# Kernel tuning notes

Measured on AMD Instinct MI355X. Metric: run time of the kernel, lower is better.

## Reference

```python
import jax, jax.numpy as jnp
import numpy as np

HIND = 512
D = 256
P = 512          # 2*d Givens rotations
RHO_MAX = 9.0
DELTA = 1e-3
EPS = 1e-8
B = 32768


def setup_inputs() -> dict:
    key = jax.random.key(0)
    ks = jax.random.split(key, 12)
    f = lambda k, shape, sc=1.0: jax.random.normal(k, shape, dtype=jnp.float32) * sc
    return {
        "ent_embed": f(ks[0], (B, HIND)),
        "rel_embed": f(ks[1], (B, HIND)),
        "ent_label": f(ks[2], (B, HIND)),
        "sim": jax.random.uniform(ks[3], (B,), dtype=jnp.float32),
        # W_v: Linear(hind, d)
        "Wv": f(ks[4], (D, HIND), 0.05), "bv": jnp.zeros((D,), jnp.float32),
        # w_rho_ent: Linear(hind, 1), bias init 0.5
        "Wre": f(ks[5], (1, HIND), 0.05), "bre": jnp.full((1,), 0.5, jnp.float32),
        # w_rho_rel: Linear(hind, 1)
        "Wrr": f(ks[6], (1, HIND), 0.05), "brr": jnp.zeros((1,), jnp.float32),
        # W_theta: Linear(hind, P)
        "Wt": f(ks[7], (P, HIND), 0.05), "bt": jnp.zeros((P,), jnp.float32),
        "ga_rho": jnp.array([2.0], jnp.float32), "gb_rho": jnp.array([-0.5], jnp.float32),
        "ga_phi": jnp.array([2.0], jnp.float32), "gb_phi": jnp.array([-0.5], jnp.float32),
        # pre_mlp: Linear(hind,hind) -> ReLU -> Linear(hind,hind)
        "W1": f(ks[8], (HIND, HIND), 0.03), "b1": jnp.zeros((HIND,), jnp.float32),
        "W2": f(ks[9], (HIND, HIND), 0.03), "b2": jnp.zeros((HIND,), jnp.float32),
    }


def _l2norm(x):
    return x / (jnp.linalg.norm(x, axis=1, keepdims=True) + EPS)


def _forward(ent_embed, rel_embed, ent_label, sim,
             Wv, bv, Wre, bre, Wrr, brr, Wt, bt,
             ga_rho, gb_rho, ga_phi, gb_phi, W1, b1, W2, b2):
    pre = lambda x: x + jax.nn.relu(x @ W1.T + b1) @ W2.T + b2  # residual pre_mlp
    E_h, E_r, E_t = pre(ent_embed), pre(rel_embed), pre(ent_label)

    def to_polar(E):
        u = _l2norm(E @ Wv.T + bv)                       # [B, D] direction
        rho = jax.nn.softplus(E @ Wre.T + bre)           # [B, 1] radius
        return jnp.clip(rho, 0.0, RHO_MAX), u

    rho_h, u_h = to_polar(E_h)
    delta_rho = E_r @ Wrr.T + brr                        # [B, 1]
    thetas = jnp.pi * jnp.tanh(E_r @ Wt.T + bt)          # [B, P]

    simc = sim.reshape(-1, 1)
    g_rho = jax.nn.sigmoid(ga_rho * simc + gb_rho)
    g_phi = jax.nn.sigmoid(ga_phi * simc + gb_phi)
    rho_prime = jnp.clip(rho_h + delta_rho * g_rho, 0.0, RHO_MAX)

    # Sequential Givens rotations: pairs (m % D, (m % D + 1) % D)
    ii = jnp.arange(P, dtype=jnp.int32) % D
    jj = (ii + 1) % D
    c = jnp.cos(thetas).T                                # [P, B]
    s = jnp.sin(thetas).T

    def step(out, t):
        i, j, cm, sm = t
        ui, uj = out[:, i], out[:, j]
        out = out.at[:, i].set(cm * ui - sm * uj)
        out = out.at[:, j].set(sm * ui + cm * uj)
        return out, None

    u_rot, _ = jax.lax.scan(step, u_h, (ii, jj, c, s))
    u_rot = _l2norm(u_rot)

    # slerp(u_h -> u_rot, alpha = g_phi), lerp fallback when omega <= DELTA
    dot = jnp.clip(jnp.sum(u_h * u_rot, axis=1, keepdims=True), -1.0 + EPS, 1.0 - EPS)
    omega = jnp.arccos(dot)
    sin_omega = jnp.sin(omega)
    mask = (omega > DELTA).astype(u_h.dtype)
    s1 = jnp.sin((1.0 - g_phi) * omega) / (sin_omega + EPS)
    s2 = jnp.sin(g_phi * omega) / (sin_omega + EPS)
    u_prime = mask * (s1 * u_h + s2 * u_rot) + (1.0 - mask) * ((1.0 - g_phi) * u_h + g_phi * u_rot)
    u_prime = _l2norm(u_prime)

    rho_t, u_t = to_polar(E_t)
    # Lorentz lift: X = [cosh(rho), sinh(rho)*u]; inner = -x0*y0 + <xs, ys>
    Xh0, Xhs = jnp.cosh(rho_prime), jnp.sinh(rho_prime) * u_prime
    Xt0, Xts = jnp.cosh(rho_t), jnp.sinh(rho_t) * u_t
    score = (-Xh0 * Xt0 + jnp.sum(Xhs * Xts, axis=1, keepdims=True))[:, 0]  # [B]
    return score


def reference(ent_embed, rel_embed, ent_label, sim,
              Wv, bv, Wre, bre, Wrr, brr, Wt, bt,
              ga_rho, gb_rho, ga_phi, gb_phi, W1, b1, W2, b2):
    return _forward(ent_embed, rel_embed, ent_label, sim,
                    Wv, bv, Wre, bre, Wrr, brr, Wt, bt,
                    ga_rho, gb_rho, ga_phi, gb_phi, W1, b1, W2, b2)
```

## Files before the change

kernel.cpp:

```cpp
#include <hip/hip_runtime.h>
#include <cstdint>

#define NB 32768
#define HH 512

typedef __attribute__((ext_vector_type(8))) _Float16 f16x8;
typedef __attribute__((ext_vector_type(4))) float f32x4;
typedef __attribute__((ext_vector_type(4))) unsigned short us4v;

__device__ __forceinline__ unsigned short f2h(float f) {
  _Float16 h = (_Float16)f;
  return __builtin_bit_cast(unsigned short, h);
}
__device__ __forceinline__ float h2f(unsigned short u) {
  return (float)__builtin_bit_cast(_Float16, u);
}

__device__ __forceinline__ void gl_lds16(const void* g, void* l) {
  __builtin_amdgcn_global_load_lds(
      (const __attribute__((address_space(1))) unsigned int*)g,
      (__attribute__((address_space(3))) unsigned int*)l, 16, 0, 0);
}

__device__ __forceinline__ float wred(float v) {
#pragma unroll
  for (int off = 32; off > 0; off >>= 1) v += __shfl_xor(v, off);
  return v;
}

__device__ __forceinline__ float softplusf(float x) {
  return fmaxf(x, 0.f) + log1pf(expf(-fabsf(x)));
}

__global__ __launch_bounds__(256) void prep_w(
    const float* __restrict__ W1, const float* __restrict__ W2,
    const float* __restrict__ Wv, const float* __restrict__ Wt,
    unsigned short* __restrict__ W1h, unsigned short* __restrict__ W2h,
    unsigned short* __restrict__ Wvh, unsigned short* __restrict__ Wth,
    float* __restrict__ rho) {
  int i = blockIdx.x * 256 + threadIdx.x;
  if (i < 98304) rho[i] = 0.f;
  if (i < 262144) W1h[i] = f2h(W1[i]);
  else if (i < 524288) W2h[i - 262144] = f2h(W2[i - 262144]);
  else if (i < 655360) Wvh[i - 524288] = f2h(Wv[i - 524288]);
  else Wth[i - 655360] = f2h(Wt[i - 655360]);
}

__global__ __launch_bounds__(256) void gemm0_k(
    const float* __restrict__ A, const unsigned short* __restrict__ W,
    const float* __restrict__ bias, unsigned short* __restrict__ Out) {
  __shared__ float Af[128 * 64];
  __shared__ unsigned short Bs[128 * 64];
  const int tid = threadIdx.x, lane = tid & 63, w = tid >> 6;
  const long m0 = (long)blockIdx.y * 128;
  const int n0 = blockIdx.x * 128;
  const int wr = (w >> 1) * 64, wc = (w & 1) * 64;

  const int arow = w * 32 + (lane >> 4), acol = (lane & 15) * 4;
  const float* Ag = A + (long)(m0 + arow) * HH + acol;
  float* Al = Af + arow * 64 + acol;
  const int brow = w * 32 + (lane >> 3), bcol = (lane & 7) * 8;
  const unsigned short* Bg = W + (long)(n0 + brow) * HH + bcol;
  unsigned short* Bl = Bs + brow * 64 + bcol;

  f32x4 acc[4][4] = {};
  for (int kb = 0; kb < 8; ++kb) {
    const int ko = kb * 64;
#pragma unroll
    for (int q = 0; q < 8; ++q)
      gl_lds16(Ag + (long)(4 * q) * HH + ko, Al + (4 * q) * 64);
#pragma unroll
    for (int q = 0; q < 4; ++q)
      gl_lds16(Bg + (long)(8 * q) * HH + ko, Bl + (8 * q) * 64);
    __syncthreads();
#pragma unroll
    for (int ks = 0; ks < 2; ++ks) {
      const int kcol = ks * 32 + (lane >> 4) * 8;
      f16x8 af[4], bf[4];
#pragma unroll
      for (int i = 0; i < 4; ++i) {
        const float* ap = Af + (wr + i * 16 + (lane & 15)) * 64 + kcol;
        f32x4 a0 = *(const f32x4*)ap;
        f32x4 a1 = *(const f32x4*)(ap + 4);
        f16x8 t;
        t[0] = (_Float16)a0[0]; t[1] = (_Float16)a0[1];
        t[2] = (_Float16)a0[2]; t[3] = (_Float16)a0[3];
        t[4] = (_Float16)a1[0]; t[5] = (_Float16)a1[1];
        t[6] = (_Float16)a1[2]; t[7] = (_Float16)a1[3];
        af[i] = t;
        bf[i] = *(const f16x8*)(Bs + (wc + i * 16 + (lane & 15)) * 64 + kcol);
      }
#pragma unroll
      for (int i = 0; i < 4; ++i)
#pragma unroll
        for (int j = 0; j < 4; ++j)
          acc[i][j] = __builtin_amdgcn_mfma_f32_16x16x32_f16(af[i], bf[j], acc[i][j], 0, 0, 0);
    }
    __syncthreads();
  }

  const int cg = lane >> 4, cl = lane & 15;
#pragma unroll
  for (int mi = 0; mi < 4; ++mi) {
    const long row0 = m0 + wr + mi * 16 + cg * 4;
#pragma unroll
    for (int ni = 0; ni < 4; ++ni) {
      const int col = n0 + wc + ni * 16 + cl;
      const float bcol = bias[col];
#pragma unroll
      for (int r = 0; r < 4; ++r)
        Out[(row0 + r) * HH + col] = f2h(fmaxf(acc[mi][ni][r] + bcol, 0.f));
    }
  }
}

template <int MODE>
__global__ __launch_bounds__(256) void gemm16_k(
    const unsigned short* __restrict__ A, const unsigned short* __restrict__ W,
    const float* __restrict__ bias, const float* __restrict__ Xres,
    const float* __restrict__ wsel, float* __restrict__ rho_base,
    unsigned short* __restrict__ OutH, float* __restrict__ OutF, int ldo) {
  __shared__ unsigned short As[128 * 64];
  __shared__ unsigned short Bs[128 * 64];
  const int tid = threadIdx.x, lane = tid & 63, w = tid >> 6;
  const long m0 = (long)blockIdx.y * 128;
  const int n0 = blockIdx.x * 128;
  const int wr = (w >> 1) * 64, wc = (w & 1) * 64;

  const int srow = w * 32 + (lane >> 3), scol = (lane & 7) * 8;
  const unsigned short* Ag = A + (long)(m0 + srow) * HH + scol;
  const unsigned short* Bg = W + (long)(n0 + srow) * HH + scol;
  unsigned short* Al = As + srow * 64 + scol;
  unsigned short* Bl = Bs + srow * 64 + scol;

  f32x4 acc[4][4] = {};
  for (int kb = 0; kb < 8; ++kb) {
    const int ko = kb * 64;
#pragma unroll
    for (int q = 0; q < 4; ++q) {
      gl_lds16(Ag + (long)(8 * q) * HH + ko, Al + (8 * q) * 64);
      gl_lds16(Bg + (long)(8 * q) * HH + ko, Bl + (8 * q) * 64);
    }
    __syncthreads();
#pragma unroll
    for (int ks = 0; ks < 2; ++ks) {
      const int kcol = ks * 32 + (lane >> 4) * 8;
      f16x8 af[4], bf[4];
#pragma unroll
      for (int i = 0; i < 4; ++i) {
        af[i] = *(const f16x8*)(As + (wr + i * 16 + (lane & 15)) * 64 + kcol);
        bf[i] = *(const f16x8*)(Bs + (wc + i * 16 + (lane & 15)) * 64 + kcol);
      }
#pragma unroll
      for (int i = 0; i < 4; ++i)
#pragma unroll
        for (int j = 0; j < 4; ++j)
          acc[i][j] = __builtin_amdgcn_mfma_f32_16x16x32_f16(af[i], bf[j], acc[i][j], 0, 0, 0);
    }
    __syncthreads();
  }

  const int cg = lane >> 4, cl = lane & 15;
  float drow[4][4] = {};
#pragma unroll
  for (int mi = 0; mi < 4; ++mi) {
    const long row0 = m0 + wr + mi * 16 + cg * 4;
#pragma unroll
    for (int ni = 0; ni < 4; ++ni) {
      const int col = n0 + wc + ni * 16 + cl;
      const float bcol = bias[col];
      float wv = 0.f;
      if constexpr (MODE == 1) wv = wsel[col];
#pragma unroll
      for (int r = 0; r < 4; ++r) {
        const long row = row0 + r;
        float v = acc[mi][ni][r] + bcol;
        if constexpr (MODE == 1) {
          v += Xres[row * HH + col];
          OutH[row * HH + col] = f2h(v);
          drow[mi][r] += v * wv;
        } else if constexpr (MODE == 2) {
          OutH[row * (long)ldo + col] = f2h(v);
        } else {
          OutF[row * (long)ldo + col] = v;
        }
      }
    }
  }
  if constexpr (MODE == 1) {
#pragma unroll
    for (int mi = 0; mi < 4; ++mi)
#pragma unroll
      for (int r = 0; r < 4; ++r) {
        float s = drow[mi][r];
        s += __shfl_xor(s, 1);
        s += __shfl_xor(s, 2);
        s += __shfl_xor(s, 4);
        s += __shfl_xor(s, 8);
        if (cl == 0) atomicAdd(&rho_base[m0 + wr + mi * 16 + cg * 4 + r], s);
      }
  }
}

__device__ __forceinline__ void givens_pass(float v[4], const float c[4],
                                            const float s[4], int lane) {
  float vn3 = __shfl_down(v[0], 1);
  float A = 1.f, Bc = 0.f;
#pragma unroll
  for (int k = 0; k < 4; ++k) {
    float vnext = (k < 3) ? v[k + 1] : vn3;
    bool skip = (lane == 63) && (k == 3);
    if (!skip) {
      Bc = s[k] * Bc + c[k] * vnext;
      A = s[k] * A;
    }
  }
  float iA = A, iB = Bc;
#pragma unroll
  for (int off = 1; off < 64; off <<= 1) {
    float pA = __shfl_up(iA, off);
    float pB = __shfl_up(iB, off);
    if (lane >= off) { iB = iA * pB + iB; iA = iA * pA; }
  }
  float eA = __shfl_up(iA, 1);
  float eB = __shfl_up(iB, 1);
  if (lane == 0) { eA = 1.f; eB = 0.f; }
  float v0g = __shfl(v[0], 0);
  float K = eA * v0g + eB;
  float out[4];
#pragma unroll
  for (int k = 0; k < 4; ++k) {
    float vnext = (k < 3) ? v[k + 1] : vn3;
    bool skip = (lane == 63) && (k == 3);
    if (!skip) {
      out[k] = c[k] * K - s[k] * vnext;
      K = s[k] * K + c[k] * vnext;
    } else out[k] = 0.f;
  }
  float K255 = __shfl(K, 63);
  float c255 = __shfl(c[3], 63);
  float s255 = __shfl(s[3], 63);
  float o0 = __shfl(out[0], 0);
  if (lane == 63) out[3] = c255 * K255 - s255 * o0;
  if (lane == 0) out[0] = s255 * K255 + c255 * o0;
  v[0] = out[0]; v[1] = out[1]; v[2] = out[2]; v[3] = out[3];
}

__global__ __launch_bounds__(256) void final_k(
    const unsigned short* __restrict__ Uh, const unsigned short* __restrict__ Ut,
    const float* __restrict__ TH, const float* __restrict__ rho_raw,
    const float* __restrict__ sim, const float* __restrict__ bre,
    const float* __restrict__ brr, const float* __restrict__ ga_rho,
    const float* __restrict__ gb_rho, const float* __restrict__ ga_phi,
    const float* __restrict__ gb_phi, float* __restrict__ out) {
  const int lane = threadIdx.x & 63;
  const int b = blockIdx.x * 4 + (threadIdx.x >> 6);

  us4v h4 = *(const us4v*)(Uh + (long)b * 256 + lane * 4);
  us4v t4 = *(const us4v*)(Ut + (long)b * 256 + lane * 4);
  const float* th = TH + (long)b * 512;
  f32x4 tA = *(const f32x4*)(th + lane * 4);
  f32x4 tB = *(const f32x4*)(th + 256 + lane * 4);

  float vh[4], vt[4];
#pragma unroll
  for (int k = 0; k < 4; ++k) { vh[k] = h2f(h4[k]); vt[k] = h2f(t4[k]); }

  const float PI_F = 3.14159265358979f;
  float cA[4], sA[4], cB[4], sB[4];
#pragma unroll
  for (int k = 0; k < 4; ++k) {
    float a1 = PI_F * tanhf(tA[k]);
    sincosf(a1, &sA[k], &cA[k]);
    float a2 = PI_F * tanhf(tB[k]);
    sincosf(a2, &sB[k], &cB[k]);
  }

  float ssq = wred(vh[0] * vh[0] + vh[1] * vh[1] + vh[2] * vh[2] + vh[3] * vh[3]);
  float invh = 1.f / (sqrtf(ssq) + 1e-8f);
  float u[4], v[4];
#pragma unroll
  for (int k = 0; k < 4; ++k) { u[k] = vh[k] * invh; v[k] = u[k]; }

  givens_pass(v, cA, sA, lane);
  givens_pass(v, cB, sB, lane);

  float ssr = wred(v[0] * v[0] + v[1] * v[1] + v[2] * v[2] + v[3] * v[3]);
  float invr = 1.f / (sqrtf(ssr) + 1e-8f);
  float ur[4];
#pragma unroll
  for (int k = 0; k < 4; ++k) ur[k] = v[k] * invr;

  float dt = wred(u[0] * ur[0] + u[1] * ur[1] + u[2] * ur[2] + u[3] * ur[3]);
  dt = fminf(fmaxf(dt, -1.f + 1e-8f), 1.f - 1e-8f);
  float omega = acosf(dt);
  float sino = sinf(omega);
  float sb = sim[b];
  float gphi = 1.f / (1.f + expf(-(ga_phi[0] * sb + gb_phi[0])));
  float s1, s2;
  if (omega > 0.001f) {
    s1 = sinf((1.f - gphi) * omega) / (sino + 1e-8f);
    s2 = sinf(gphi * omega) / (sino + 1e-8f);
  } else {
    s1 = 1.f - gphi;
    s2 = gphi;
  }
  float up[4];
#pragma unroll
  for (int k = 0; k < 4; ++k) up[k] = s1 * u[k] + s2 * ur[k];
  float ssp = wred(up[0] * up[0] + up[1] * up[1] + up[2] * up[2] + up[3] * up[3]);
  float invp = 1.f / (sqrtf(ssp) + 1e-8f);
  float sst = wred(vt[0] * vt[0] + vt[1] * vt[1] + vt[2] * vt[2] + vt[3] * vt[3]);
  float invt = 1.f / (sqrtf(sst) + 1e-8f);
  float dp = wred(up[0] * vt[0] + up[1] * vt[1] + up[2] * vt[2] + up[3] * vt[3]) * invp * invt;

  float rh = fminf(fmaxf(softplusf(rho_raw[b] + bre[0]), 0.f), 9.f);
  float rt = fminf(fmaxf(softplusf(rho_raw[NB + b] + bre[0]), 0.f), 9.f);
  float dR = rho_raw[2 * NB + b] + brr[0];
  float grho = 1.f / (1.f + expf(-(ga_rho[0] * sb + gb_rho[0])));
  float rp = fminf(fmaxf(rh + dR * grho, 0.f), 9.f);
  float score = -coshf(rp) * coshf(rt) + sinhf(rp) * sinhf(rt) * dp;
  if (lane == 0) out[b] = score;
}

extern "C" void kernel_launch(void* const* d_in, const int* in_sizes, int n_in,
                              void* d_out, int out_size, void* d_ws, size_t ws_size,
                              hipStream_t stream) {
  (void)in_sizes; (void)n_in;
  const float* ent = (const float*)d_in[0];
  const float* rel = (const float*)d_in[1];
  const float* lab = (const float*)d_in[2];
  const float* sim = (const float*)d_in[3];
  const float* Wv = (const float*)d_in[4];
  const float* bv = (const float*)d_in[5];
  const float* Wre = (const float*)d_in[6];
  const float* bre = (const float*)d_in[7];
  const float* Wrr = (const float*)d_in[8];
  const float* brr = (const float*)d_in[9];
  const float* Wt = (const float*)d_in[10];
  const float* bt = (const float*)d_in[11];
  const float* ga_rho = (const float*)d_in[12];
  const float* gb_rho = (const float*)d_in[13];
  const float* ga_phi = (const float*)d_in[14];
  const float* gb_phi = (const float*)d_in[15];
  const float* W1 = (const float*)d_in[16];
  const float* b1 = (const float*)d_in[17];
  const float* W2 = (const float*)d_in[18];
  const float* b2 = (const float*)d_in[19];

  const size_t NEEDED = 170000384ULL;
  if (ws_size < NEEDED) {
    (void)hipMemsetAsync(d_out, 0, (size_t)out_size * sizeof(float), stream);
    return;
  }
  char* ws = (char*)d_ws;
  float* TH = (float*)ws;
  unsigned short* Uh = (unsigned short*)(ws + 67108864);
  unsigned short* Ut = (unsigned short*)(ws + 83886080);
  unsigned short* Tb = (unsigned short*)(ws + 100663296);
  unsigned short* Eb = (unsigned short*)(ws + 134217728);
  float* rho_raw = (float*)(ws + 167772160);
  unsigned short* W1h = (unsigned short*)(ws + 168165376);
  unsigned short* W2h = (unsigned short*)(ws + 168689664);
  unsigned short* Wvh = (unsigned short*)(ws + 169213952);
  unsigned short* Wth = (unsigned short*)(ws + 169476096);

  prep_w<<<dim3(3584), dim3(256), 0, stream>>>(W1, W2, Wv, Wt, W1h, W2h, Wvh, Wth, rho_raw);

  gemm0_k<<<dim3(4, 256), dim3(256), 0, stream>>>(ent, W1h, b1, Tb);
  gemm16_k<1><<<dim3(4, 256), dim3(256), 0, stream>>>(
      Tb, W2h, b2, ent, Wre, rho_raw, Eb, nullptr, HH);
  gemm16_k<2><<<dim3(2, 256), dim3(256), 0, stream>>>(
      Eb, Wvh, bv, nullptr, nullptr, nullptr, Uh, nullptr, 256);

  gemm0_k<<<dim3(4, 256), dim3(256), 0, stream>>>(lab, W1h, b1, Tb);
  gemm16_k<1><<<dim3(4, 256), dim3(256), 0, stream>>>(
      Tb, W2h, b2, lab, Wre, rho_raw + NB, Eb, nullptr, HH);
  gemm16_k<2><<<dim3(2, 256), dim3(256), 0, stream>>>(
      Eb, Wvh, bv, nullptr, nullptr, nullptr, Ut, nullptr, 256);

  gemm0_k<<<dim3(4, 256), dim3(256), 0, stream>>>(rel, W1h, b1, Tb);
  gemm16_k<1><<<dim3(4, 256), dim3(256), 0, stream>>>(
      Tb, W2h, b2, rel, Wrr, rho_raw + 2 * NB, Eb, nullptr, HH);
  gemm16_k<3><<<dim3(4, 256), dim3(256), 0, stream>>>(
      Eb, Wth, bt, nullptr, nullptr, nullptr, nullptr, TH, HH);

  final_k<<<dim3(8192), dim3(256), 0, stream>>>(
      Uh, Ut, TH, rho_raw, sim, bre, brr, ga_rho, gb_rho, ga_phi, gb_phi, (float*)d_out);
}
```

Measured before the change: 605.1 us.

## Fold W2 into downstream projections and batch all three entities per launch

The residual pre-MLP's second GEMM is folded algebraically into the heads. The new code precomputes Wv·W2, Wt·W2 and Wre/Wrr·W2, so the heads consume the raw input plus the ReLU hidden state as one concatenated K=1024 GEMM. The radius projections are split into a raw-input dot product and a hidden-state dot product, both done inside the first GEMM, and all three entities are batched into one launch per stage. The goal is to drop a full 512x512 GEMM per entity, the intermediate E buffer writes and reads, and several launches. The theta buffer moves to fp16 and fast intrinsics replace the transcendental functions, at some cost in accuracy. M2t reuses W1h's memory after gemm1, which relies on stream ordering.

```diff
diff --git a/kernel.cpp b/kernel.cpp
--- a/kernel.cpp
+++ b/kernel.cpp
@@ -8,86 +8,128 @@
 typedef __attribute__((ext_vector_type(4))) float f32x4;
 typedef __attribute__((ext_vector_type(4))) unsigned short us4v;
 
-__device__ __forceinline__ unsigned short f2h(float f) {
+static __device__ __forceinline__ unsigned short f2h(float f) {
   _Float16 h = (_Float16)f;
   return __builtin_bit_cast(unsigned short, h);
 }
-__device__ __forceinline__ float h2f(unsigned short u) {
+static __device__ __forceinline__ float h2f(unsigned short u) {
   return (float)__builtin_bit_cast(_Float16, u);
 }
-
-__device__ __forceinline__ void gl_lds16(const void* g, void* l) {
+static __device__ __forceinline__ void gl_lds16(const void* g, void* l) {
   __builtin_amdgcn_global_load_lds(
       (const __attribute__((address_space(1))) unsigned int*)g,
       (__attribute__((address_space(3))) unsigned int*)l, 16, 0, 0);
 }
-
-__device__ __forceinline__ float wred(float v) {
+static __device__ __forceinline__ float wred(float v) {
 #pragma unroll
   for (int off = 32; off > 0; off >>= 1) v += __shfl_xor(v, off);
   return v;
 }
-
-__device__ __forceinline__ float softplusf(float x) {
-  return fmaxf(x, 0.f) + log1pf(expf(-fabsf(x)));
-}
-
-__global__ __launch_bounds__(256) void prep_w(
-    const float* __restrict__ W1, const float* __restrict__ W2,
-    const float* __restrict__ Wv, const float* __restrict__ Wt,
-    unsigned short* __restrict__ W1h, unsigned short* __restrict__ W2h,
-    unsigned short* __restrict__ Wvh, unsigned short* __restrict__ Wth,
-    float* __restrict__ rho) {
-  int i = blockIdx.x * 256 + threadIdx.x;
-  if (i < 98304) rho[i] = 0.f;
-  if (i < 262144) W1h[i] = f2h(W1[i]);
-  else if (i < 524288) W2h[i - 262144] = f2h(W2[i - 262144]);
-  else if (i < 655360) Wvh[i - 524288] = f2h(Wv[i - 524288]);
-  else Wth[i - 655360] = f2h(Wt[i - 655360]);
-}
-
-__global__ __launch_bounds__(256) void gemm0_k(
-    const float* __restrict__ A, const unsigned short* __restrict__ W,
-    const float* __restrict__ bias, unsigned short* __restrict__ Out) {
+static __device__ __forceinline__ float sigm(float x) { return 1.f / (1.f + __expf(-x)); }
+static __device__ __forceinline__ float tanh_fast(float x) {
+  return 1.f - 2.f / (__expf(2.f * x) + 1.f);
+}
+static __device__ __forceinline__ float softplus_fast(float x) {
+  return fmaxf(x, 0.f) + log1pf(__expf(-fabsf(x)));
+}
+
+__global__ __launch_bounds__(256) void prep_k(
+    const float* __restrict__ W1, const float* __restrict__ Wv,
+    const float* __restrict__ Wt, const float* __restrict__ Wre,
+    const float* __restrict__ Wrr, const float* __restrict__ b2,
+    const float* __restrict__ W2,
+    unsigned short* __restrict__ W1h, unsigned short* __restrict__ Wvh,
+    unsigned short* __restrict__ Wth, float* __restrict__ rho_raw,
+    float* __restrict__ w2re, float* __restrict__ w2rr, float* __restrict__ rho_c) {
+  __shared__ float red[4];
+  const int bx = blockIdx.x, t = threadIdx.x;
+  if (bx < 2560) {
+    int i = bx * 256 + t;
+    if (i < 98304) rho_raw[i] = 0.f;
+    if (i < 262144) W1h[i] = f2h(W1[i]);
+    else if (i < 393216) Wvh[i - 262144] = f2h(Wv[i - 262144]);
+    else Wth[i - 393216] = f2h(Wt[i - 393216]);
+  } else if (bx < 2562) {
+    const float* ws = (bx == 2560) ? Wre : Wrr;
+    float* wd = (bx == 2560) ? w2re : w2rr;
+    float a0 = 0.f, a1 = 0.f;
+    for (int j = 0; j < 512; ++j) {
+      float wv = ws[j];
+      a0 += wv * W2[j * 512 + t];
+      a1 += wv * W2[j * 512 + t + 256];
+    }
+    wd[t] = a0;
+    wd[t + 256] = a1;
+  } else {
+    const float* ws = (bx == 2562) ? Wre : Wrr;
+    float p = b2[t] * ws[t] + b2[t + 256] * ws[t + 256];
+    p = wred(p);
+    if ((t & 63) == 0) red[t >> 6] = p;
+    __syncthreads();
+    if (t == 0) rho_c[bx - 2562] = red[0] + red[1] + red[2] + red[3];
+  }
+}
+
+__global__ __launch_bounds__(256, 3) void gemm1_k(
+    const float* __restrict__ x0, const float* __restrict__ x1,
+    const float* __restrict__ x2, const unsigned short* __restrict__ W1h,
+    const float* __restrict__ b1, const float* __restrict__ wre,
+    const float* __restrict__ wrr, const float* __restrict__ w2re,
+    const float* __restrict__ w2rr, unsigned short* __restrict__ Tbig,
+    float* __restrict__ rho_raw) {
   __shared__ float Af[128 * 64];
   __shared__ unsigned short Bs[128 * 64];
   const int tid = threadIdx.x, lane = tid & 63, w = tid >> 6;
-  const long m0 = (long)blockIdx.y * 128;
+  const int by = blockIdx.y, ent = by >> 8;
+  const long mloc = (long)(by & 255) * 128;
+  const float* X = (ent == 0) ? x0 : (ent == 1) ? x1 : x2;
+  const float* wsel = (ent < 2) ? wre : wrr;
+  const float* w2sel = (ent < 2) ? w2re : w2rr;
   const int n0 = blockIdx.x * 128;
+  const bool do_rx = (blockIdx.x == 0) && ((w & 1) == 0);
   const int wr = (w >> 1) * 64, wc = (w & 1) * 64;
 
   const int arow = w * 32 + (lane >> 4), acol = (lane & 15) * 4;
-  const float* Ag = A + (long)(m0 + arow) * HH + acol;
+  const float* Ag = X + (mloc + arow) * HH + acol;
   float* Al = Af + arow * 64 + acol;
   const int brow = w * 32 + (lane >> 3), bcol = (lane & 7) * 8;
-  const unsigned short* Bg = W + (long)(n0 + brow) * HH + bcol;
+  const unsigned short* Bg = W1h + (long)(n0 + brow) * HH + bcol;
   unsigned short* Bl = Bs + brow * 64 + bcol;
 
   f32x4 acc[4][4] = {};
+  float rx[4] = {0.f, 0.f, 0.f, 0.f};
   for (int kb = 0; kb < 8; ++kb) {
     const int ko = kb * 64;
 #pragma unroll
-    for (int q = 0; q < 8; ++q)
-      gl_lds16(Ag + (long)(4 * q) * HH + ko, Al + (4 * q) * 64);
-#pragma unroll
-    for (int q = 0; q < 4; ++q)
-      gl_lds16(Bg + (long)(8 * q) * HH + ko, Bl + (8 * q) * 64);
+    for (int q = 0; q < 8; ++q) gl_lds16(Ag + (long)(4 * q) * HH + ko, Al + (4 * q) * 64);
+#pragma unroll
+    for (int q = 0; q < 4; ++q) gl_lds16(Bg + (long)(8 * q) * HH + ko, Bl + (8 * q) * 64);
     __syncthreads();
 #pragma unroll
     for (int ks = 0; ks < 2; ++ks) {
       const int kcol = ks * 32 + (lane >> 4) * 8;
+      float wv[8];
+      if (do_rx) {
+        f32x4 wa = *(const f32x4*)(wsel + ko + kcol);
+        f32x4 wb = *(const f32x4*)(wsel + ko + kcol + 4);
+        wv[0] = wa[0]; wv[1] = wa[1]; wv[2] = wa[2]; wv[3] = wa[3];
+        wv[4] = wb[0]; wv[5] = wb[1]; wv[6] = wb[2]; wv[7] = wb[3];
+      }
       f16x8 af[4], bf[4];
 #pragma unroll
       for (int i = 0; i < 4; ++i) {
         const float* ap = Af + (wr + i * 16 + (lane & 15)) * 64 + kcol;
-        f32x4 a0 = *(const f32x4*)ap;
-        f32x4 a1 = *(const f32x4*)(ap + 4);
+        f32x4 a0 = *(const f32x4*)ap, a1 = *(const f32x4*)(ap + 4);
         f16x8 t;
         t[0] = (_Float16)a0[0]; t[1] = (_Float16)a0[1];
         t[2] = (_Float16)a0[2]; t[3] = (_Float16)a0[3];
         t[4] = (_Float16)a1[0]; t[5] = (_Float16)a1[1];
         t[6] = (_Float16)a1[2]; t[7] = (_Float16)a1[3];
         af[i] = t;
+        if (do_rx) {
+          rx[i] += a0[0] * wv[0] + a0[1] * wv[1] + a0[2] * wv[2] + a0[3] * wv[3] +
+                   a1[0] * wv[4] + a1[1] * wv[5] + a1[2] * wv[6] + a1[3] * wv[7];
+        }
         bf[i] = *(const f16x8*)(Bs + (wc + i * 16 + (lane & 15)) * 64 + kcol);
       }
 #pragma unroll
@@ -100,47 +142,120 @@
   }
 
   const int cg = lane >> 4, cl = lane & 15;
+  const long rbase = (long)ent * NB + mloc;
+  float drow[4][4] = {};
 #pragma unroll
   for (int mi = 0; mi < 4; ++mi) {
-    const long row0 = m0 + wr + mi * 16 + cg * 4;
+    const long row0 = rbase + wr + mi * 16 + cg * 4;
 #pragma unroll
     for (int ni = 0; ni < 4; ++ni) {
       const int col = n0 + wc + ni * 16 + cl;
-      const float bcol = bias[col];
-#pragma unroll
-      for (int r = 0; r < 4; ++r)
-        Out[(row0 + r) * HH + col] = f2h(fmaxf(acc[mi][ni][r] + bcol, 0.f));
-    }
-  }
-}
-
-template <int MODE>
-__global__ __launch_bounds__(256) void gemm16_k(
-    const unsigned short* __restrict__ A, const unsigned short* __restrict__ W,
-    const float* __restrict__ bias, const float* __restrict__ Xres,
-    const float* __restrict__ wsel, float* __restrict__ rho_base,
-    unsigned short* __restrict__ OutH, float* __restrict__ OutF, int ldo) {
-  __shared__ unsigned short As[128 * 64];
+      const float bc = b1[col], w2v = w2sel[col];
+#pragma unroll
+      for (int r = 0; r < 4; ++r) {
+        float v = fmaxf(acc[mi][ni][r] + bc, 0.f);
+        Tbig[(row0 + r) * HH + col] = f2h(v);
+        drow[mi][r] += v * w2v;
+      }
+    }
+  }
+#pragma unroll
+  for (int mi = 0; mi < 4; ++mi)
+#pragma unroll
+    for (int r = 0; r < 4; ++r) {
+      float s = drow[mi][r];
+      s += __shfl_xor(s, 1); s += __shfl_xor(s, 2);
+      s += __shfl_xor(s, 4); s += __shfl_xor(s, 8);
+      if (cl == 0) atomicAdd(&rho_raw[rbase + wr + mi * 16 + cg * 4 + r], s);
+    }
+  if (do_rx) {
+#pragma unroll
+    for (int i = 0; i < 4; ++i) {
+      float s = rx[i];
+      s += __shfl_xor(s, 16); s += __shfl_xor(s, 32);
+      if (lane < 16) atomicAdd(&rho_raw[rbase + wr + i * 16 + lane], s);
+    }
+  }
+}
+
+__global__ __launch_bounds__(256) void m2_k(
+    const float* __restrict__ Wv, const float* __restrict__ Wt,
+    const float* __restrict__ W2, const float* __restrict__ b2,
+    const float* __restrict__ bv, const float* __restrict__ bt,
+    unsigned short* __restrict__ M2v, unsigned short* __restrict__ M2t,
+    float* __restrict__ bcv, float* __restrict__ bct) {
+  __shared__ float rowL[512];
+  __shared__ float red[4];
+  const int b = blockIdx.x, t = threadIdx.x;
+  int n; const float* src; unsigned short* dst; const float* badd; float* bdst;
+  if (b < 256) { n = b; src = Wv + (long)n * 512; dst = M2v + (long)n * 512; badd = bv; bdst = bcv; }
+  else { n = b - 256; src = Wt + (long)n * 512; dst = M2t + (long)n * 512; badd = bt; bdst = bct; }
+  rowL[t] = src[t]; rowL[t + 256] = src[t + 256];
+  __syncthreads();
+  float a0 = 0.f, a1 = 0.f;
+  for (int j = 0; j < 512; ++j) {
+    float rv = rowL[j];
+    a0 += rv * W2[(long)j * 512 + t];
+    a1 += rv * W2[(long)j * 512 + t + 256];
+  }
+  dst[t] = f2h(a0);
+  dst[t + 256] = f2h(a1);
+  float p = b2[t] * rowL[t] + b2[t + 256] * rowL[t + 256];
+  p = wred(p);
+  if ((t & 63) == 0) red[t >> 6] = p;
+  __syncthreads();
+  if (t == 0) bdst[n] = badd[n] + red[0] + red[1] + red[2] + red[3];
+}
+
+__global__ __launch_bounds__(256, 3) void head_k(
+    const float* __restrict__ x0, const float* __restrict__ x1,
+    const float* __restrict__ x2, const unsigned short* __restrict__ Tbig,
+    const unsigned short* __restrict__ Wvh, const unsigned short* __restrict__ Wth,
+    const unsigned short* __restrict__ M2v, const unsigned short* __restrict__ M2t,
+    const float* __restrict__ bcv, const float* __restrict__ bct,
+    unsigned short* __restrict__ Uh, unsigned short* __restrict__ Ut,
+    unsigned short* __restrict__ THh) {
+  __shared__ float Af[128 * 64];
   __shared__ unsigned short Bs[128 * 64];
+  unsigned short* As16 = (unsigned short*)Af;
   const int tid = threadIdx.x, lane = tid & 63, w = tid >> 6;
-  const long m0 = (long)blockIdx.y * 128;
-  const int n0 = blockIdx.x * 128;
+  const int bx = blockIdx.x;
+  int ent, n0, ldo; long mloc;
+  const float* X; const unsigned short *Wx, *Wm; const float* bias; unsigned short* Out;
+  if (bx < 1024) {
+    int nt = bx & 1, mt = bx >> 1;
+    ent = mt >> 8; mloc = (long)(mt & 255) * 128; n0 = nt * 128; ldo = 256;
+    X = ent ? x1 : x0; Wx = Wvh; Wm = M2v; bias = bcv; Out = ent ? Ut : Uh;
+  } else {
+    int t = bx - 1024, nt = t & 3, mt = t >> 2;
+    ent = 2; mloc = (long)mt * 128; n0 = nt * 128; ldo = 512;
+    X = x2; Wx = Wth; Wm = M2t; bias = bct; Out = THh;
+  }
+  const long trow = (long)ent * NB + mloc;
   const int wr = (w >> 1) * 64, wc = (w & 1) * 64;
 
+  const int arow = w * 32 + (lane >> 4), acol = (lane & 15) * 4;
+  const float* Ag = X + (mloc + arow) * HH + acol;
+  float* Al = Af + arow * 64 + acol;
   const int srow = w * 32 + (lane >> 3), scol = (lane & 7) * 8;
-  const unsigned short* Ag = A + (long)(m0 + srow) * HH + scol;
-  const unsigned short* Bg = W + (long)(n0 + srow) * HH + scol;
-  unsigned short* Al = As + srow * 64 + scol;
-  unsigned short* Bl = Bs + srow * 64 + scol;
+  const unsigned short* Tg = Tbig + (trow + srow) * HH + scol;
+  unsigned short* Sl = As16 + srow * 64 + scol;
+  const int brow = srow, bcol = scol;
+  unsigned short* Bl = Bs + brow * 64 + bcol;
 
   f32x4 acc[4][4] = {};
-  for (int kb = 0; kb < 8; ++kb) {
-    const int ko = kb * 64;
-#pragma unroll
-    for (int q = 0; q < 4; ++q) {
-      gl_lds16(Ag + (long)(8 * q) * HH + ko, Al + (8 * q) * 64);
-      gl_lds16(Bg + (long)(8 * q) * HH + ko, Bl + (8 * q) * 64);
-    }
+  for (int kb = 0; kb < 16; ++kb) {
+    const int ko = (kb & 7) * 64;
+    if (kb < 8) {
+#pragma unroll
+      for (int q = 0; q < 8; ++q) gl_lds16(Ag + (long)(4 * q) * HH + ko, Al + (4 * q) * 64);
+    } else {
+#pragma unroll
+      for (int q = 0; q < 4; ++q) gl_lds16(Tg + (long)(8 * q) * HH + ko, Sl + (8 * q) * 64);
+    }
+    const unsigned short* Bg = ((kb < 8) ? Wx : Wm) + (long)(n0 + brow) * HH + bcol;
+#pragma unroll
+    for (int q = 0; q < 4; ++q) gl_lds16(Bg + (long)(8 * q) * HH + ko, Bl + (8 * q) * 64);
     __syncthreads();
 #pragma unroll
     for (int ks = 0; ks < 2; ++ks) {
@@ -148,7 +263,18 @@
       f16x8 af[4], bf[4];
 #pragma unroll
       for (int i = 0; i < 4; ++i) {
-        af[i] = *(const f16x8*)(As + (wr + i * 16 + (lane & 15)) * 64 + kcol);
+        if (kb < 8) {
+          const float* ap = Af + (wr + i * 16 + (lane & 15)) * 64 + kcol;
+          f32x4 a0 = *(const f32x4*)ap, a1 = *(const f32x4*)(ap + 4);
+          f16x8 t;
+          t[0] = (_Float16)a0[0]; t[1] = (_Float16)a0[1];
+          t[2] = (_Float16)a0[2]; t[3] = (_Float16)a0[3];
+          t[4] = (_Float16)a1[0]; t[5] = (_Float16)a1[1];
+          t[6] = (_Float16)a1[2]; t[7] = (_Float16)a1[3];
+          af[i] = t;
+        } else {
+          af[i] = *(const f16x8*)(As16 + (wr + i * 16 + (lane & 15)) * 64 + kcol);
+        }
         bf[i] = *(const f16x8*)(Bs + (wc + i * 16 + (lane & 15)) * 64 + kcol);
       }
 #pragma unroll
@@ -161,44 +287,17 @@
   }
 
   const int cg = lane >> 4, cl = lane & 15;
-  float drow[4][4] = {};
 #pragma unroll
   for (int mi = 0; mi < 4; ++mi) {
-    const long row0 = m0 + wr + mi * 16 + cg * 4;
+    const long row0 = mloc + wr + mi * 16 + cg * 4;
 #pragma unroll
     for (int ni = 0; ni < 4; ++ni) {
       const int col = n0 + wc + ni * 16 + cl;
-      const float bcol = bias[col];
-      float wv = 0.f;
-      if constexpr (MODE == 1) wv = wsel[col];
-#pragma unroll
-      for (int r = 0; r < 4; ++r) {
-        const long row = row0 + r;
-        float v = acc[mi][ni][r] + bcol;
-        if constexpr (MODE == 1) {
-          v += Xres[row * HH + col];
-          OutH[row * HH + col] = f2h(v);
-          drow[mi][r] += v * wv;
-        } else if constexpr (MODE == 2) {
-          OutH[row * (long)ldo + col] = f2h(v);
-        } else {
-          OutF[row * (long)ldo + col] = v;
-        }
-      }
-    }
-  }
-  if constexpr (MODE == 1) {
-#pragma unroll
-    for (int mi = 0; mi < 4; ++mi)
-#pragma unroll
-      for (int r = 0; r < 4; ++r) {
-        float s = drow[mi][r];
-        s += __shfl_xor(s, 1);
-        s += __shfl_xor(s, 2);
-        s += __shfl_xor(s, 4);
-        s += __shfl_xor(s, 8);
-        if (cl == 0) atomicAdd(&rho_base[m0 + wr + mi * 16 + cg * 4 + r], s);
-      }
+      const float bc = bias[col];
+#pragma unroll
+      for (int r = 0; r < 4; ++r)
+        Out[(row0 + r) * (long)ldo + col] = f2h(acc[mi][ni][r] + bc);
+    }
   }
 }
 
@@ -210,10 +309,7 @@
   for (int k = 0; k < 4; ++k) {
     float vnext = (k < 3) ? v[k + 1] : vn3;
     bool skip = (lane == 63) && (k == 3);
-    if (!skip) {
-      Bc = s[k] * Bc + c[k] * vnext;
-      A = s[k] * A;
-    }
+    if (!skip) { Bc = s[k] * Bc + c[k] * vnext; A = s[k] * A; }
   }
   float iA = A, iB = Bc;
 #pragma unroll
@@ -248,32 +344,29 @@
 
 __global__ __launch_bounds__(256) void final_k(
     const unsigned short* __restrict__ Uh, const unsigned short* __restrict__ Ut,
-    const float* __restrict__ TH, const float* __restrict__ rho_raw,
-    const float* __restrict__ sim, const float* __restrict__ bre,
-    const float* __restrict__ brr, const float* __restrict__ ga_rho,
-    const float* __restrict__ gb_rho, const float* __restrict__ ga_phi,
-    const float* __restrict__ gb_phi, float* __restrict__ out) {
+    const unsigned short* __restrict__ THh, const float* __restrict__ rho_raw,
+    const float* __restrict__ rho_c, const float* __restrict__ sim,
+    const float* __restrict__ bre, const float* __restrict__ brr,
+    const float* __restrict__ ga_rho, const float* __restrict__ gb_rho,
+    const float* __restrict__ ga_phi, const float* __restrict__ gb_phi,
+    float* __restrict__ out) {
   const int lane = threadIdx.x & 63;
   const int b = blockIdx.x * 4 + (threadIdx.x >> 6);
 
   us4v h4 = *(const us4v*)(Uh + (long)b * 256 + lane * 4);
   us4v t4 = *(const us4v*)(Ut + (long)b * 256 + lane * 4);
-  const float* th = TH + (long)b * 512;
-  f32x4 tA = *(const f32x4*)(th + lane * 4);
-  f32x4 tB = *(const f32x4*)(th + 256 + lane * 4);
-
-  float vh[4], vt[4];
-#pragma unroll
-  for (int k = 0; k < 4; ++k) { vh[k] = h2f(h4[k]); vt[k] = h2f(t4[k]); }
+  us4v a4 = *(const us4v*)(THh + (long)b * 512 + lane * 4);
+  us4v b4 = *(const us4v*)(THh + (long)b * 512 + 256 + lane * 4);
 
   const float PI_F = 3.14159265358979f;
-  float cA[4], sA[4], cB[4], sB[4];
+  float vh[4], vt[4], cA[4], sA[4], cB[4], sB[4];
 #pragma unroll
   for (int k = 0; k < 4; ++k) {
-    float a1 = PI_F * tanhf(tA[k]);
-    sincosf(a1, &sA[k], &cA[k]);
-    float a2 = PI_F * tanhf(tB[k]);
-    sincosf(a2, &sB[k], &cB[k]);
+    vh[k] = h2f(h4[k]); vt[k] = h2f(t4[k]);
+    float aa = PI_F * tanh_fast(h2f(a4[k]));
+    sA[k] = __sinf(aa); cA[k] = __cosf(aa);
+    float ab = PI_F * tanh_fast(h2f(b4[k]));
+    sB[k] = __sinf(ab); cB[k] = __cosf(ab);
   }
 
   float ssq = wred(vh[0] * vh[0] + vh[1] * vh[1] + vh[2] * vh[2] + vh[3] * vh[3]);
@@ -294,13 +387,13 @@
   float dt = wred(u[0] * ur[0] + u[1] * ur[1] + u[2] * ur[2] + u[3] * ur[3]);
   dt = fminf(fmaxf(dt, -1.f + 1e-8f), 1.f - 1e-8f);
   float omega = acosf(dt);
-  float sino = sinf(omega);
+  float sino = sqrtf(fmaxf(1.f - dt * dt, 0.f));
   float sb = sim[b];
-  float gphi = 1.f / (1.f + expf(-(ga_phi[0] * sb + gb_phi[0])));
+  float gphi = sigm(ga_phi[0] * sb + gb_phi[0]);
   float s1, s2;
   if (omega > 0.001f) {
-    s1 = sinf((1.f - gphi) * omega) / (sino + 1e-8f);
-    s2 = sinf(gphi * omega) / (sino + 1e-8f);
+    s1 = __sinf((1.f - gphi) * omega) / (sino + 1e-8f);
+    s2 = __sinf(gphi * omega) / (sino + 1e-8f);
   } else {
     s1 = 1.f - gphi;
     s2 = gphi;
@@ -314,12 +407,14 @@
   float invt = 1.f / (sqrtf(sst) + 1e-8f);
   float dp = wred(up[0] * vt[0] + up[1] * vt[1] + up[2] * vt[2] + up[3] * vt[3]) * invp * invt;
 
-  float rh = fminf(fmaxf(softplusf(rho_raw[b] + bre[0]), 0.f), 9.f);
-  float rt = fminf(fmaxf(softplusf(rho_raw[NB + b] + bre[0]), 0.f), 9.f);
-  float dR = rho_raw[2 * NB + b] + brr[0];
-  float grho = 1.f / (1.f + expf(-(ga_rho[0] * sb + gb_rho[0])));
+  float rh = fminf(fmaxf(softplus_fast(rho_raw[b] + rho_c[0] + bre[0]), 0.f), 9.f);
+  float rt = fminf(fmaxf(softplus_fast(rho_raw[NB + b] + rho_c[0] + bre[0]), 0.f), 9.f);
+  float dR = rho_raw[2 * NB + b] + rho_c[1] + brr[0];
+  float grho = sigm(ga_rho[0] * sb + gb_rho[0]);
   float rp = fminf(fmaxf(rh + dR * grho, 0.f), 9.f);
-  float score = -coshf(rp) * coshf(rt) + sinhf(rp) * sinhf(rt) * dp;
+  float er = __expf(rp), eri = __expf(-rp);
+  float et = __expf(rt), eti = __expf(-rt);
+  float score = -0.25f * (er + eri) * (et + eti) + 0.25f * (er - eri) * (et - eti) * dp;
   if (lane == 0) out[b] = score;
 }
 
@@ -327,9 +422,9 @@
                               void* d_out, int out_size, void* d_ws, size_t ws_size,
                               hipStream_t stream) {
   (void)in_sizes; (void)n_in;
-  const float* ent = (const float*)d_in[0];
-  const float* rel = (const float*)d_in[1];
-  const float* lab = (const float*)d_in[2];
+  const float* x0 = (const float*)d_in[0];
+  const float* x2 = (const float*)d_in[1];
+  const float* x1 = (const float*)d_in[2];
   const float* sim = (const float*)d_in[3];
   const float* Wv = (const float*)d_in[4];
   const float* bv = (const float*)d_in[5];
@@ -348,43 +443,40 @@
   const float* W2 = (const float*)d_in[18];
   const float* b2 = (const float*)d_in[19];
 
-  const size_t NEEDED = 170000384ULL;
+  const size_t NEEDED = 169745416ULL;
   if (ws_size < NEEDED) {
     (void)hipMemsetAsync(d_out, 0, (size_t)out_size * sizeof(float), stream);
     return;
   }
   char* ws = (char*)d_ws;
-  float* TH = (float*)ws;
-  unsigned short* Uh = (unsigned short*)(ws + 67108864);
-  unsigned short* Ut = (unsigned short*)(ws + 83886080);
-  unsigned short* Tb = (unsigned short*)(ws + 100663296);
-  unsigned short* Eb = (unsigned short*)(ws + 134217728);
+  unsigned short* Tbig = (unsigned short*)ws;
+  unsigned short* Uh = (unsigned short*)(ws + 100663296);
+  unsigned short* Ut = (unsigned short*)(ws + 117440512);
+  unsigned short* THh = (unsigned short*)(ws + 134217728);
   float* rho_raw = (float*)(ws + 167772160);
   unsigned short* W1h = (unsigned short*)(ws + 168165376);
-  unsigned short* W2h = (unsigned short*)(ws + 168689664);
-  unsigned short* Wvh = (unsigned short*)(ws + 169213952);
-  unsigned short* Wth = (unsigned short*)(ws + 169476096);
-
-  prep_w<<<dim3(3584), dim3(256), 0, stream>>>(W1, W2, Wv, Wt, W1h, W2h, Wvh, Wth, rho_raw);
-
-  gemm0_k<<<dim3(4, 256), dim3(256), 0, stream>>>(ent, W1h, b1, Tb);
-  gemm16_k<1><<<dim3(4, 256), dim3(256), 0, stream>>>(
-      Tb, W2h, b2, ent, Wre, rho_raw, Eb, nullptr, HH);
-  gemm16_k<2><<<dim3(2, 256), dim3(256), 0, stream>>>(
-      Eb, Wvh, bv, nullptr, nullptr, nullptr, Uh, nullptr, 256);
-
-  gemm0_k<<<dim3(4, 256), dim3(256), 0, stream>>>(lab, W1h, b1, Tb);
-  gemm16_k<1><<<dim3(4, 256), dim3(256), 0, stream>>>(
-      Tb, W2h, b2, lab, Wre, rho_raw + NB, Eb, nullptr, HH);
-  gemm16_k<2><<<dim3(2, 256), dim3(256), 0, stream>>>(
-      Eb, Wvh, bv, nullptr, nullptr, nullptr, Ut, nullptr, 256);
-
-  gemm0_k<<<dim3(4, 256), dim3(256), 0, stream>>>(rel, W1h, b1, Tb);
-  gemm16_k<1><<<dim3(4, 256), dim3(256), 0, stream>>>(
-      Tb, W2h, b2, rel, Wrr, rho_raw + 2 * NB, Eb, nullptr, HH);
-  gemm16_k<3><<<dim3(4, 256), dim3(256), 0, stream>>>(
-      Eb, Wth, bt, nullptr, nullptr, nullptr, nullptr, TH, HH);
+  unsigned short* Wvh = (unsigned short*)(ws + 168689664);
+  unsigned short* Wth = (unsigned short*)(ws + 168951808);
+  unsigned short* M2v = (unsigned short*)(ws + 169476096);
+  unsigned short* M2t = W1h;
+  float* w2re = (float*)(ws + 169738240);
+  float* w2rr = (float*)(ws + 169740288);
+  float* bcv = (float*)(ws + 169742336);
+  float* bct = (float*)(ws + 169743360);
+  float* rho_c = (float*)(ws + 169745408);
+
+  prep_k<<<dim3(2564), dim3(256), 0, stream>>>(
+      W1, Wv, Wt, Wre, Wrr, b2, W2, W1h, Wvh, Wth, rho_raw, w2re, w2rr, rho_c);
+
+  gemm1_k<<<dim3(4, 768), dim3(256), 0, stream>>>(
+      x0, x1, x2, W1h, b1, Wre, Wrr, w2re, w2rr, Tbig, rho_raw);
+
+  m2_k<<<dim3(768), dim3(256), 0, stream>>>(Wv, Wt, W2, b2, bv, bt, M2v, M2t, bcv, bct);
+
+  head_k<<<dim3(2048), dim3(256), 0, stream>>>(
+      x0, x1, x2, Tbig, Wvh, Wth, M2v, M2t, bcv, bct, Uh, Ut, THh);
 
   final_k<<<dim3(8192), dim3(256), 0, stream>>>(
-      Uh, Ut, TH, rho_raw, sim, bre, brr, ga_rho, gb_rho, ga_phi, gb_phi, (float*)d_out);
-}
+      Uh, Ut, THh, rho_raw, rho_c, sim, bre, brr, ga_rho, gb_rho, ga_phi, gb_phi,
+      (float*)d_out);
+}
```

After: 594.8 us. Within noise of the previous version (-1.7%).
